# Kernel tuning notes

Measured on AMD Instinct MI355X. Metric: run time of the kernel, lower is better.

Reference implementation:

```python
import jax, jax.numpy as jnp
import numpy as np

D_MODEL = 512
HEADS = 8
CTX = 2048
BATCH = 4
SEQ = 2048


def make_rotary_matrix(context_window, d):
    # Faithful to the source, including theta = 10000 ** (-2*(i-1)/d)
    i = np.arange(d // 2)
    theta = 10000.0 ** (-2.0 * (i - 1) / d)  # [d/2]
    pos = np.arange(context_window)
    m_theta = pos[:, None] * theta[None, :]  # [m, d/2]
    cos, sin = np.cos(m_theta), np.sin(m_theta)
    R = np.zeros((context_window, d, d), dtype=np.float32)
    even, odd = 2 * i, 2 * i + 1
    R[:, even, even] = cos
    R[:, even, odd] = -sin
    R[:, odd, even] = sin
    R[:, odd, odd] = cos
    return jnp.asarray(R)


def setup_inputs() -> dict:
    key = jax.random.key(0)
    ks = jax.random.split(key, 8)
    s = 1.0 / np.sqrt(D_MODEL)
    x = jax.random.normal(ks[0], (BATCH, SEQ, D_MODEL), dtype=jnp.float32)
    Wq = jax.random.normal(ks[1], (D_MODEL, D_MODEL), dtype=jnp.float32) * s
    Wk = jax.random.normal(ks[2], (D_MODEL, D_MODEL), dtype=jnp.float32) * s
    Wv = jax.random.normal(ks[3], (D_MODEL, D_MODEL), dtype=jnp.float32) * s
    in_proj_w = jax.random.normal(ks[4], (3 * D_MODEL, D_MODEL), dtype=jnp.float32) * s
    in_proj_b = jax.random.normal(ks[5], (3 * D_MODEL,), dtype=jnp.float32) * 0.01
    out_w = jax.random.normal(ks[6], (D_MODEL, D_MODEL), dtype=jnp.float32) * s
    out_b = jax.random.normal(ks[7], (D_MODEL,), dtype=jnp.float32) * 0.01
    R = make_rotary_matrix(CTX, D_MODEL)
    return {"x": x, "Wq": Wq, "Wk": Wk, "Wv": Wv, "R": R,
            "in_proj_w": in_proj_w, "in_proj_b": in_proj_b,
            "out_w": out_w, "out_b": out_b}


def reference(x, Wq, Wk, Wv, R, in_proj_w, in_proj_b, out_w, out_b):
    b, m, d = x.shape
    h = HEADS
    hd = d // h
    # outer QKV projections (bias=False)
    q = x @ Wq.T
    k = x @ Wk.T
    v = x @ Wv.T
    # dense per-position rotary rotation: q_out[b,p,:] = q[b,p,:] @ R[p]
    Rm = R[:m]
    q = jnp.einsum('bmd,mde->bme', q, Rm)
    k = jnp.einsum('bmd,mde->bme', k, Rm)
    v = jnp.einsum('bmd,mde->bme', v, Rm)
    # nn.MultiheadAttention in_proj (bias=True) -- dropout skipped (eval)
    wq_i, wk_i, wv_i = jnp.split(in_proj_w, 3, axis=0)
    bq, bk, bv = jnp.split(in_proj_b, 3, axis=0)
    qp = (q @ wq_i.T + bq).reshape(b, m, h, hd).transpose(0, 2, 1, 3)
    kp = (k @ wk_i.T + bk).reshape(b, m, h, hd).transpose(0, 2, 1, 3)
    vp = (v @ wv_i.T + bv).reshape(b, m, h, hd).transpose(0, 2, 1, 3)
    scale = 1.0 / np.sqrt(hd)
    scores = jnp.einsum('bhqd,bhkd->bhqk', qp, kp) * scale
    causal = jnp.triu(jnp.full((m, m), -jnp.inf, dtype=scores.dtype), k=1)
    attn = jax.nn.softmax(scores + causal, axis=-1)
    out = jnp.einsum('bhqk,bhkd->bhqd', attn, vp)
    out = out.transpose(0, 2, 1, 3).reshape(b, m, d)
    return out @ out_w.T + out_b
```

## Files before the change

kernel.cpp:

```cpp
#include <hip/hip_runtime.h>
#include <cmath>

typedef unsigned short u16;
typedef __bf16 bf16x8 __attribute__((ext_vector_type(8)));
typedef float f32x4 __attribute__((ext_vector_type(4)));

#define SEQL 2048
#define NH 8
#define HD 64
#define MROWS 8192

static __device__ __forceinline__ u16 f2bf(float f) {
  union { float f; unsigned u; } v; v.f = f;
  unsigned u = v.u;
  unsigned r = (u + 0x7FFFu + ((u >> 16) & 1u)) >> 16;
  return (u16)r;
}

static __device__ __forceinline__ void cvt4(const float* __restrict__ in,
                                            u16* __restrict__ out, int lb) {
  int i = lb * 1024 + threadIdx.x * 4;
  float4 f = *(const float4*)(in + i);
  ushort4 o;
  o.x = f2bf(f.x); o.y = f2bf(f.y); o.z = f2bf(f.z); o.w = f2bf(f.w);
  *(ushort4*)(out + i) = o;
}

__global__ __launch_bounds__(256) void prep_kernel(
    const float* __restrict__ x,  const float* __restrict__ Wq,
    const float* __restrict__ Wk, const float* __restrict__ Wv,
    const float* __restrict__ ipw, const float* __restrict__ ow,
    u16* __restrict__ xb, u16* __restrict__ Wcatb, u16* __restrict__ ipwb,
    u16* __restrict__ owb, float2* __restrict__ T) {
  int b = blockIdx.x;
  if (b < 4096)      cvt4(x,   xb,                 b);
  else if (b < 4352) cvt4(Wq,  Wcatb,              b - 4096);
  else if (b < 4608) cvt4(Wk,  Wcatb + 262144,     b - 4352);
  else if (b < 4864) cvt4(Wv,  Wcatb + 524288,     b - 4608);
  else if (b < 5632) cvt4(ipw, ipwb,               b - 4864);
  else if (b < 5888) cvt4(ow,  owb,                b - 5632);
  else {
    int idx = (b - 5888) * 256 + threadIdx.x;
    int m = idx >> 8, i = idx & 255;
    double theta = pow(10000.0, -2.0 * ((double)i - 1.0) / 512.0);
    double a = (double)m * theta;
    T[idx] = make_float2((float)cos(a), (float)sin(a));
  }
}

template<int MODE>
__global__ __launch_bounds__(256) void gemm_bt(const u16* __restrict__ A, int lda,
                                               const u16* __restrict__ B, int ldb,
                                               const float* __restrict__ bias,
                                               void* __restrict__ Cv, int ldc,
                                               const float2* __restrict__ T) {
  __shared__ u16 As[128 * 80];
  __shared__ u16 Bs[128 * 80];
  int tid = threadIdx.x;
  int wid = tid >> 6, lane = tid & 63, quad = lane >> 4, l16 = lane & 15;
  int m0 = blockIdx.y * 128, n0 = blockIdx.x * 128;
  int wm = (wid >> 1) * 64, wn = (wid & 1) * 64;
  f32x4 acc[4][4] = {};
  for (int kb = 0; kb < 512; kb += 64) {
    #pragma unroll
    for (int s = 0; s < 4; ++s) {
      int slot = tid + s * 256;
      int row = slot >> 3, sg = slot & 7;
      *(uint4*)(&As[row * 80 + sg * 8]) =
          *(const uint4*)(A + (size_t)(m0 + row) * lda + kb + sg * 8);
      *(uint4*)(&Bs[row * 80 + sg * 8]) =
          *(const uint4*)(B + (size_t)(n0 + row) * ldb + kb + sg * 8);
    }
    __syncthreads();
    #pragma unroll
    for (int kk = 0; kk < 2; ++kk) {
      bf16x8 af[4], bfr[4];
      #pragma unroll
      for (int i = 0; i < 4; ++i)
        af[i] = *(const bf16x8*)(&As[(wm + 16 * i + l16) * 80 + quad * 8 + kk * 32]);
      #pragma unroll
      for (int j = 0; j < 4; ++j)
        bfr[j] = *(const bf16x8*)(&Bs[(wn + 16 * j + l16) * 80 + quad * 8 + kk * 32]);
      #pragma unroll
      for (int i = 0; i < 4; ++i)
        #pragma unroll
        for (int j = 0; j < 4; ++j)
          acc[i][j] = __builtin_amdgcn_mfma_f32_16x16x32_bf16(af[i], bfr[j], acc[i][j], 0, 0, 0);
    }
    __syncthreads();
  }
  float sgn = (l16 & 1) ? -1.f : 1.f;
  #pragma unroll
  for (int i = 0; i < 4; ++i)
    #pragma unroll
    for (int j = 0; j < 4; ++j)
      #pragma unroll
      for (int r = 0; r < 4; ++r) {
        int row = m0 + wm + 16 * i + quad * 4 + r;
        int col = n0 + wn + 16 * j + l16;
        float v = acc[i][j][r];
        if (MODE == 3) {
          float partner = __shfl_xor(v, 1, 64);
          float2 cs = T[(row & 2047) * 256 + ((col & 511) >> 1)];
          v = v * cs.x + sgn * partner * cs.y;
          ((u16*)Cv)[(size_t)row * ldc + col] = f2bf(v);
        } else {
          v += bias[col];
          ((float*)Cv)[(size_t)row * ldc + col] = v;
        }
      }
}

__global__ __launch_bounds__(256) void gemm_inproj(const u16* __restrict__ Aall,
                                                   const u16* __restrict__ B,
                                                   const float* __restrict__ bias,
                                                   u16* __restrict__ qkvh) {
  __shared__ u16 As[128 * 80];
  __shared__ u16 Bs[128 * 80];
  int tid = threadIdx.x;
  int wid = tid >> 6, lane = tid & 63, quad = lane >> 4, l16 = lane & 15;
  int m0 = blockIdx.y * 128, n0 = blockIdx.x * 128;
  int qseg = n0 >> 9;
  const u16* A = Aall + qseg * 512;
  int wm = (wid >> 1) * 64, wn = (wid & 1) * 64;
  f32x4 acc[4][4] = {};
  for (int kb = 0; kb < 512; kb += 64) {
    #pragma unroll
    for (int s = 0; s < 4; ++s) {
      int slot = tid + s * 256;
      int row = slot >> 3, sg = slot & 7;
      *(uint4*)(&As[row * 80 + sg * 8]) =
          *(const uint4*)(A + (size_t)(m0 + row) * 1536 + kb + sg * 8);
      *(uint4*)(&Bs[row * 80 + sg * 8]) =
          *(const uint4*)(B + (size_t)(n0 + row) * 512 + kb + sg * 8);
    }
    __syncthreads();
    #pragma unroll
    for (int kk = 0; kk < 2; ++kk) {
      bf16x8 af[4], bfr[4];
      #pragma unroll
      for (int i = 0; i < 4; ++i)
        af[i] = *(const bf16x8*)(&As[(wm + 16 * i + l16) * 80 + quad * 8 + kk * 32]);
      #pragma unroll
      for (int j = 0; j < 4; ++j)
        bfr[j] = *(const bf16x8*)(&Bs[(wn + 16 * j + l16) * 80 + quad * 8 + kk * 32]);
      #pragma unroll
      for (int i = 0; i < 4; ++i)
        #pragma unroll
        for (int j = 0; j < 4; ++j)
          acc[i][j] = __builtin_amdgcn_mfma_f32_16x16x32_bf16(af[i], bfr[j], acc[i][j], 0, 0, 0);
    }
    __syncthreads();
  }
  #pragma unroll
  for (int i = 0; i < 4; ++i)
    #pragma unroll
    for (int j = 0; j < 4; ++j)
      #pragma unroll
      for (int r = 0; r < 4; ++r) {
        int row = m0 + wm + 16 * i + quad * 4 + r;
        int col = n0 + wn + 16 * j + l16;
        float v = acc[i][j][r] + bias[col];
        int cl = col & 511;
        int h = cl >> 6, dd = cl & 63;
        int bb = row >> 11, mm = row & 2047;
        if (qseg < 2) {
          qkvh[(size_t)qseg * MROWS * 512 +
               (((size_t)(bb * NH + h)) * SEQL + mm) * HD + dd] = f2bf(v);
        } else {
          qkvh[(size_t)2 * MROWS * 512 +
               ((size_t)(bb * NH + h) * HD + dd) * SEQL + mm] = f2bf(v);
        }
      }
}

static __device__ __forceinline__ f32x4 mfma_bf16(bf16x8 a, bf16x8 b, f32x4 c) {
  return __builtin_amdgcn_mfma_f32_16x16x32_bf16(a, b, c, 0, 0, 0);
}

static __device__ __forceinline__ void attn_tile(
    bf16x8 qf0, bf16x8 qf1, f32x4* o_acc, float* m_i, float* l_i,
    const u16* Ks, const u16* Vt, u16* Pw, bool diag, int wrow, int quad, int l16) {
  f32x4 s_acc[4] = {};
  #pragma unroll
  for (int j = 0; j < 4; ++j) {
    bf16x8 bk0 = *(const bf16x8*)(&Ks[(j * 16 + l16) * 80 + quad * 8]);
    bf16x8 bk1 = *(const bf16x8*)(&Ks[(j * 16 + l16) * 80 + quad * 8 + 32]);
    s_acc[j] = mfma_bf16(qf0, bk0, s_acc[j]);
    s_acc[j] = mfma_bf16(qf1, bk1, s_acc[j]);
  }
  #pragma unroll
  for (int j = 0; j < 4; ++j)
    #pragma unroll
    for (int r = 0; r < 4; ++r) {
      float sv = s_acc[j][r] * 0.125f;
      if (diag && (j * 16 + l16 > wrow + quad * 4 + r)) sv = -__builtin_inff();
      s_acc[j][r] = sv;
    }
  float p[4][4], alpha[4];
  #pragma unroll
  for (int r = 0; r < 4; ++r) {
    float mx = fmaxf(fmaxf(s_acc[0][r], s_acc[1][r]), fmaxf(s_acc[2][r], s_acc[3][r]));
    #pragma unroll
    for (int off = 1; off < 16; off <<= 1) mx = fmaxf(mx, __shfl_xor(mx, off, 64));
    float m_new = fmaxf(m_i[r], mx);
    alpha[r] = __expf(m_i[r] - m_new);
    float rs = 0.f;
    #pragma unroll
    for (int j = 0; j < 4; ++j) { float pv = __expf(s_acc[j][r] - m_new); p[j][r] = pv; rs += pv; }
    #pragma unroll
    for (int off = 1; off < 16; off <<= 1) rs += __shfl_xor(rs, off, 64);
    l_i[r] = l_i[r] * alpha[r] + rs;
    m_i[r] = m_new;
  }
  #pragma unroll
  for (int j = 0; j < 4; ++j)
    #pragma unroll
    for (int r = 0; r < 4; ++r) o_acc[j][r] *= alpha[r];
  #pragma unroll
  for (int j = 0; j < 4; ++j)
    #pragma unroll
    for (int r = 0; r < 4; ++r)
      Pw[(quad * 4 + r) * 80 + j * 16 + l16] = f2bf(p[j][r]);
  bf16x8 pf0 = *(const bf16x8*)(&Pw[l16 * 80 + quad * 8]);
  bf16x8 pf1 = *(const bf16x8*)(&Pw[l16 * 80 + quad * 8 + 32]);
  #pragma unroll
  for (int j = 0; j < 4; ++j) {
    bf16x8 bv0 = *(const bf16x8*)(&Vt[(j * 16 + l16) * 80 + quad * 8]);
    bf16x8 bv1 = *(const bf16x8*)(&Vt[(j * 16 + l16) * 80 + quad * 8 + 32]);
    o_acc[j] = mfma_bf16(pf0, bv0, o_acc[j]);
    o_acc[j] = mfma_bf16(pf1, bv1, o_acc[j]);
  }
}

__global__ __launch_bounds__(256) void flash_kernel(const u16* __restrict__ Q,
                                                    const u16* __restrict__ K,
                                                    const u16* __restrict__ Vt_g,
                                                    u16* __restrict__ O) {
  __shared__ u16 Ks[64 * 80];
  __shared__ u16 Vt[64 * 80];
  __shared__ u16 Ps[4 * 16 * 80];
  int tid = threadIdx.x;
  int wid = tid >> 6, lane = tid & 63, quad = lane >> 4, l16 = lane & 15;
  int bh = blockIdx.y;
  int b = bh >> 3, h = bh & 7;
  int q0 = blockIdx.x * 128;
  const u16* Qb = Q + (size_t)bh * SEQL * HD;
  const u16* Kb = K + (size_t)bh * SEQL * HD;
  const u16* Vb = Vt_g + (size_t)bh * HD * SEQL;
  u16* Pw = &Ps[wid * 16 * 80];

  int rowA = q0 + wid * 16 + l16;
  int rowB = rowA + 64;
  bf16x8 qA0 = *(const bf16x8*)(Qb + (size_t)rowA * HD + quad * 8);
  bf16x8 qA1 = *(const bf16x8*)(Qb + (size_t)rowA * HD + quad * 8 + 32);
  bf16x8 qB0 = *(const bf16x8*)(Qb + (size_t)rowB * HD + quad * 8);
  bf16x8 qB1 = *(const bf16x8*)(Qb + (size_t)rowB * HD + quad * 8 + 32);

  f32x4 oA[4] = {}, oB[4] = {};
  float mA[4], lA[4], mB[4], lB[4];
  #pragma unroll
  for (int r = 0; r < 4; ++r) {
    mA[r] = -__builtin_inff(); lA[r] = 0.f;
    mB[r] = -__builtin_inff(); lB[r] = 0.f;
  }

  int nkb = q0 / 64 + 2;
  for (int kb = 0; kb < nkb; ++kb) {
    int k0 = kb * 64;
    #pragma unroll
    for (int s = 0; s < 2; ++s) {
      int slot = tid + s * 256;
      int row = slot >> 3, sg = slot & 7;
      *(uint4*)(&Ks[row * 80 + sg * 8]) =
          *(const uint4*)(Kb + (size_t)(k0 + row) * HD + sg * 8);
      *(uint4*)(&Vt[row * 80 + sg * 8]) =
          *(const uint4*)(Vb + (size_t)row * SEQL + k0 + sg * 8);
    }
    __syncthreads();
    if (kb < nkb - 1)
      attn_tile(qA0, qA1, oA, mA, lA, Ks, Vt, Pw, kb == nkb - 2, wid * 16, quad, l16);
    attn_tile(qB0, qB1, oB, mB, lB, Ks, Vt, Pw, kb == nkb - 1, wid * 16, quad, l16);
    __syncthreads();
  }
  #pragma unroll
  for (int j = 0; j < 4; ++j)
    #pragma unroll
    for (int r = 0; r < 4; ++r) {
      int mA_idx = q0 + wid * 16 + quad * 4 + r;
      O[((size_t)(b * SEQL + mA_idx)) * 512 + h * HD + j * 16 + l16] = f2bf(oA[j][r] / lA[r]);
      int mB_idx = mA_idx + 64;
      O[((size_t)(b * SEQL + mB_idx)) * 512 + h * HD + j * 16 + l16] = f2bf(oB[j][r] / lB[r]);
    }
}

extern "C" void kernel_launch(void* const* d_in, const int* in_sizes, int n_in,
                              void* d_out, int out_size, void* d_ws, size_t ws_size,
                              hipStream_t stream) {
  const float* x   = (const float*)d_in[0];
  const float* Wq  = (const float*)d_in[1];
  const float* Wk  = (const float*)d_in[2];
  const float* Wv  = (const float*)d_in[3];
  const float* ipw = (const float*)d_in[5];
  const float* ipb = (const float*)d_in[6];
  const float* ow  = (const float*)d_in[7];
  const float* ob  = (const float*)d_in[8];
  float* out = (float*)d_out;

  char* w = (char*)d_ws;
  auto alloc = [&](size_t bytes) { void* p = w; w += bytes; return p; };
  u16* xb    = (u16*)alloc(8192UL * 512 * 2);
  u16* Wcatb = (u16*)alloc(3UL * 512 * 512 * 2);
  u16* ipwb  = (u16*)alloc(1536UL * 512 * 2);
  u16* owb   = (u16*)alloc(512UL * 512 * 2);
  u16* QKV0  = (u16*)alloc(8192UL * 1536 * 2);
  u16* qkvh  = (u16*)alloc(3UL * 8192 * 512 * 2);
  u16* Ob    = (u16*)alloc(8192UL * 512 * 2);
  float2* T  = (float2*)alloc(2048UL * 256 * sizeof(float2));

  prep_kernel<<<7936, 256, 0, stream>>>(x, Wq, Wk, Wv, ipw, ow,
                                        xb, Wcatb, ipwb, owb, T);
  gemm_bt<3><<<dim3(12, 64), 256, 0, stream>>>(xb, 512, Wcatb, 512, nullptr,
                                               QKV0, 1536, T);
  gemm_inproj<<<dim3(12, 64), 256, 0, stream>>>(QKV0, ipwb, ipb, qkvh);
  flash_kernel<<<dim3(16, 32), 256, 0, stream>>>(
      qkvh, qkvh + 8192UL * 512, qkvh + 2UL * 8192 * 512, Ob);
  gemm_bt<2><<<dim3(4, 64), 256, 0, stream>>>(Ob, 512, owb, 512, ob, out, 512, nullptr);
}
```

Before: 2.474 ms.

## Stage GEMM and attention tiles via direct global-to-LDS loads with XOR swizzle

Replaces register-staged uint4 global loads plus LDS stores with the global_load_lds builtin that writes 16-byte chunks straight into shared memory, in the GEMMs and the flash kernel. The LDS rows are now unpadded 64-element rows, and an XOR swizzle on the chunk index avoids bank conflicts in place of the old padding. The V-transpose epilogue of the in-projection now writes four consecutive bf16 values as one vector store. There is no explicit wait for the async LDS writes beyond __syncthreads, which relies on the compiler inserting the needed vmcnt waits.

```diff
diff --git a/kernel.cpp b/kernel.cpp
--- a/kernel.cpp
+++ b/kernel.cpp
@@ -9,12 +9,31 @@
 #define NH 8
 #define HD 64
 #define MROWS 8192
+
+typedef __attribute__((address_space(1))) unsigned int gu32;
+typedef __attribute__((address_space(3))) unsigned int lu32;
 
 static __device__ __forceinline__ u16 f2bf(float f) {
   union { float f; unsigned u; } v; v.f = f;
   unsigned u = v.u;
   unsigned r = (u + 0x7FFFu + ((u >> 16) & 1u)) >> 16;
   return (u16)r;
+}
+
+static __device__ __forceinline__ void gl16(const u16* g, u16* l) {
+  __builtin_amdgcn_global_load_lds((const gu32*)g, (lu32*)l, 16, 0, 0);
+}
+
+template<int ROWS>
+static __device__ __forceinline__ void stage_tile(const u16* __restrict__ gt, int ld,
+                                                  u16* lds, int wid, int lane) {
+  int rowl = lane >> 3;
+  int coff = ((lane & 7) ^ rowl) * 8;
+  #pragma unroll
+  for (int t = 0; t < ROWS / 32; ++t) {
+    int grp = t * 4 + wid;
+    gl16(gt + (size_t)(grp * 8 + rowl) * ld + coff, lds + grp * 512);
+  }
 }
 
 static __device__ __forceinline__ void cvt4(const float* __restrict__ in,
@@ -54,33 +73,28 @@
                                                const float* __restrict__ bias,
                                                void* __restrict__ Cv, int ldc,
                                                const float2* __restrict__ T) {
-  __shared__ u16 As[128 * 80];
-  __shared__ u16 Bs[128 * 80];
+  __shared__ u16 As[128 * 64];
+  __shared__ u16 Bs[128 * 64];
   int tid = threadIdx.x;
   int wid = tid >> 6, lane = tid & 63, quad = lane >> 4, l16 = lane & 15;
+  int x7 = l16 & 7;
   int m0 = blockIdx.y * 128, n0 = blockIdx.x * 128;
   int wm = (wid >> 1) * 64, wn = (wid & 1) * 64;
   f32x4 acc[4][4] = {};
   for (int kb = 0; kb < 512; kb += 64) {
-    #pragma unroll
-    for (int s = 0; s < 4; ++s) {
-      int slot = tid + s * 256;
-      int row = slot >> 3, sg = slot & 7;
-      *(uint4*)(&As[row * 80 + sg * 8]) =
-          *(const uint4*)(A + (size_t)(m0 + row) * lda + kb + sg * 8);
-      *(uint4*)(&Bs[row * 80 + sg * 8]) =
-          *(const uint4*)(B + (size_t)(n0 + row) * ldb + kb + sg * 8);
-    }
+    stage_tile<128>(A + (size_t)m0 * lda + kb, lda, As, wid, lane);
+    stage_tile<128>(B + (size_t)n0 * ldb + kb, ldb, Bs, wid, lane);
     __syncthreads();
     #pragma unroll
     for (int kk = 0; kk < 2; ++kk) {
+      int sw = ((kk * 4 + quad) ^ x7) * 8;
       bf16x8 af[4], bfr[4];
       #pragma unroll
       for (int i = 0; i < 4; ++i)
-        af[i] = *(const bf16x8*)(&As[(wm + 16 * i + l16) * 80 + quad * 8 + kk * 32]);
+        af[i] = *(const bf16x8*)(&As[(wm + 16 * i + l16) * 64 + sw]);
       #pragma unroll
       for (int j = 0; j < 4; ++j)
-        bfr[j] = *(const bf16x8*)(&Bs[(wn + 16 * j + l16) * 80 + quad * 8 + kk * 32]);
+        bfr[j] = *(const bf16x8*)(&Bs[(wn + 16 * j + l16) * 64 + sw]);
       #pragma unroll
       for (int i = 0; i < 4; ++i)
         #pragma unroll
@@ -115,35 +129,30 @@
                                                    const u16* __restrict__ B,
                                                    const float* __restrict__ bias,
                                                    u16* __restrict__ qkvh) {
-  __shared__ u16 As[128 * 80];
-  __shared__ u16 Bs[128 * 80];
+  __shared__ u16 As[128 * 64];
+  __shared__ u16 Bs[128 * 64];
   int tid = threadIdx.x;
   int wid = tid >> 6, lane = tid & 63, quad = lane >> 4, l16 = lane & 15;
+  int x7 = l16 & 7;
   int m0 = blockIdx.y * 128, n0 = blockIdx.x * 128;
   int qseg = n0 >> 9;
   const u16* A = Aall + qseg * 512;
   int wm = (wid >> 1) * 64, wn = (wid & 1) * 64;
   f32x4 acc[4][4] = {};
   for (int kb = 0; kb < 512; kb += 64) {
-    #pragma unroll
-    for (int s = 0; s < 4; ++s) {
-      int slot = tid + s * 256;
-      int row = slot >> 3, sg = slot & 7;
-      *(uint4*)(&As[row * 80 + sg * 8]) =
-          *(const uint4*)(A + (size_t)(m0 + row) * 1536 + kb + sg * 8);
-      *(uint4*)(&Bs[row * 80 + sg * 8]) =
-          *(const uint4*)(B + (size_t)(n0 + row) * 512 + kb + sg * 8);
-    }
+    stage_tile<128>(A + (size_t)m0 * 1536 + kb, 1536, As, wid, lane);
+    stage_tile<128>(B + (size_t)n0 * 512 + kb, 512, Bs, wid, lane);
     __syncthreads();
     #pragma unroll
     for (int kk = 0; kk < 2; ++kk) {
+      int sw = ((kk * 4 + quad) ^ x7) * 8;
       bf16x8 af[4], bfr[4];
       #pragma unroll
       for (int i = 0; i < 4; ++i)
-        af[i] = *(const bf16x8*)(&As[(wm + 16 * i + l16) * 80 + quad * 8 + kk * 32]);
+        af[i] = *(const bf16x8*)(&As[(wm + 16 * i + l16) * 64 + sw]);
       #pragma unroll
       for (int j = 0; j < 4; ++j)
-        bfr[j] = *(const bf16x8*)(&Bs[(wn + 16 * j + l16) * 80 + quad * 8 + kk * 32]);
+        bfr[j] = *(const bf16x8*)(&Bs[(wn + 16 * j + l16) * 64 + sw]);
       #pragma unroll
       for (int i = 0; i < 4; ++i)
         #pragma unroll
@@ -155,23 +164,28 @@
   #pragma unroll
   for (int i = 0; i < 4; ++i)
     #pragma unroll
-    for (int j = 0; j < 4; ++j)
-      #pragma unroll
-      for (int r = 0; r < 4; ++r) {
-        int row = m0 + wm + 16 * i + quad * 4 + r;
-        int col = n0 + wn + 16 * j + l16;
-        float v = acc[i][j][r] + bias[col];
-        int cl = col & 511;
-        int h = cl >> 6, dd = cl & 63;
-        int bb = row >> 11, mm = row & 2047;
-        if (qseg < 2) {
+    for (int j = 0; j < 4; ++j) {
+      int rb = m0 + wm + 16 * i + quad * 4;
+      int col = n0 + wn + 16 * j + l16;
+      float bv = bias[col];
+      int cl = col & 511;
+      int h = cl >> 6, dd = cl & 63;
+      int bb = rb >> 11;
+      if (qseg < 2) {
+        #pragma unroll
+        for (int r = 0; r < 4; ++r) {
+          int mm = (rb + r) & 2047;
           qkvh[(size_t)qseg * MROWS * 512 +
-               (((size_t)(bb * NH + h)) * SEQL + mm) * HD + dd] = f2bf(v);
-        } else {
-          qkvh[(size_t)2 * MROWS * 512 +
-               ((size_t)(bb * NH + h) * HD + dd) * SEQL + mm] = f2bf(v);
+               (((size_t)(bb * NH + h)) * SEQL + mm) * HD + dd] = f2bf(acc[i][j][r] + bv);
         }
+      } else {
+        ushort4 o;
+        o.x = f2bf(acc[i][j][0] + bv); o.y = f2bf(acc[i][j][1] + bv);
+        o.z = f2bf(acc[i][j][2] + bv); o.w = f2bf(acc[i][j][3] + bv);
+        *(ushort4*)&qkvh[(size_t)2 * MROWS * 512 +
+                         ((size_t)(bb * NH + h) * HD + dd) * SEQL + (rb & 2047)] = o;
       }
+    }
 }
 
 static __device__ __forceinline__ f32x4 mfma_bf16(bf16x8 a, bf16x8 b, f32x4 c) {
@@ -181,11 +195,14 @@
 static __device__ __forceinline__ void attn_tile(
     bf16x8 qf0, bf16x8 qf1, f32x4* o_acc, float* m_i, float* l_i,
     const u16* Ks, const u16* Vt, u16* Pw, bool diag, int wrow, int quad, int l16) {
+  int x7 = l16 & 7;
+  int sw0 = (quad ^ x7) * 8;
+  int sw1 = ((quad + 4) ^ x7) * 8;
   f32x4 s_acc[4] = {};
   #pragma unroll
   for (int j = 0; j < 4; ++j) {
-    bf16x8 bk0 = *(const bf16x8*)(&Ks[(j * 16 + l16) * 80 + quad * 8]);
-    bf16x8 bk1 = *(const bf16x8*)(&Ks[(j * 16 + l16) * 80 + quad * 8 + 32]);
+    bf16x8 bk0 = *(const bf16x8*)(&Ks[(j * 16 + l16) * 64 + sw0]);
+    bf16x8 bk1 = *(const bf16x8*)(&Ks[(j * 16 + l16) * 64 + sw1]);
     s_acc[j] = mfma_bf16(qf0, bk0, s_acc[j]);
     s_acc[j] = mfma_bf16(qf1, bk1, s_acc[j]);
   }
@@ -226,8 +243,8 @@
   bf16x8 pf1 = *(const bf16x8*)(&Pw[l16 * 80 + quad * 8 + 32]);
   #pragma unroll
   for (int j = 0; j < 4; ++j) {
-    bf16x8 bv0 = *(const bf16x8*)(&Vt[(j * 16 + l16) * 80 + quad * 8]);
-    bf16x8 bv1 = *(const bf16x8*)(&Vt[(j * 16 + l16) * 80 + quad * 8 + 32]);
+    bf16x8 bv0 = *(const bf16x8*)(&Vt[(j * 16 + l16) * 64 + sw0]);
+    bf16x8 bv1 = *(const bf16x8*)(&Vt[(j * 16 + l16) * 64 + sw1]);
     o_acc[j] = mfma_bf16(pf0, bv0, o_acc[j]);
     o_acc[j] = mfma_bf16(pf1, bv1, o_acc[j]);
   }
@@ -237,8 +254,8 @@
                                                     const u16* __restrict__ K,
                                                     const u16* __restrict__ Vt_g,
                                                     u16* __restrict__ O) {
-  __shared__ u16 Ks[64 * 80];
-  __shared__ u16 Vt[64 * 80];
+  __shared__ u16 Ks[64 * 64];
+  __shared__ u16 Vt[64 * 64];
   __shared__ u16 Ps[4 * 16 * 80];
   int tid = threadIdx.x;
   int wid = tid >> 6, lane = tid & 63, quad = lane >> 4, l16 = lane & 15;
@@ -268,15 +285,8 @@
   int nkb = q0 / 64 + 2;
   for (int kb = 0; kb < nkb; ++kb) {
     int k0 = kb * 64;
-    #pragma unroll
-    for (int s = 0; s < 2; ++s) {
-      int slot = tid + s * 256;
-      int row = slot >> 3, sg = slot & 7;
-      *(uint4*)(&Ks[row * 80 + sg * 8]) =
-          *(const uint4*)(Kb + (size_t)(k0 + row) * HD + sg * 8);
-      *(uint4*)(&Vt[row * 80 + sg * 8]) =
-          *(const uint4*)(Vb + (size_t)row * SEQL + k0 + sg * 8);
-    }
+    stage_tile<64>(Kb + (size_t)k0 * HD, HD, Ks, wid, lane);
+    stage_tile<64>(Vb + k0, SEQL, Vt, wid, lane);
     __syncthreads();
     if (kb < nkb - 1)
       attn_tile(qA0, qA1, oA, mA, lA, Ks, Vt, Pw, kb == nkb - 2, wid * 16, quad, l16);
```

After: 2.508 ms (median of 2 runs). About the same (+1.4%).
